# Optimization experiments

Measured on AMD Instinct MI355X. Metric: run time of the kernel, lower is better.

## Reference

```python
import jax, jax.numpy as jnp
import numpy as np

B, QLEN, MLEN, E, H, DH = 2, 1024, 1024, 1024, 16, 64
KLEN = QLEN + MLEN
LN_EPS = 1e-3  # keras LayerNormalization default epsilon


def layer_norm(x, gamma, beta):
    mu = jnp.mean(x, axis=-1, keepdims=True)
    var = jnp.mean(jnp.square(x - mu), axis=-1, keepdims=True)
    return (x - mu) * jax.lax.rsqrt(var + LN_EPS) * gamma + beta


def rel_shift(x):
    # x: [B, H, q, k] -> standard Transformer-XL relative shift
    b, h, q, k = x.shape
    x = jnp.pad(x, ((0, 0), (0, 0), (0, 0), (1, 0)))
    x = x.reshape(b, h, k + 1, q)[:, :, 1:, :]
    return x.reshape(b, h, q, k)


def setup_inputs() -> dict:
    key = jax.random.key(0)
    ks = jax.random.split(key, 12)
    s = 0.02
    inp = {
        "w": jax.random.normal(ks[0], (B, QLEN, E), jnp.float32),
        "r": jax.random.normal(ks[1], (1, KLEN, E), jnp.float32),
        "member": jax.random.normal(ks[2], (B, MLEN, E), jnp.float32),
        # causal mask over concatenated keys: 1 = masked
        "attn_mask": (jnp.arange(KLEN)[None, :] > (jnp.arange(QLEN)[:, None] + MLEN)).astype(jnp.float32),
        "Wq": jax.random.normal(ks[3], (E, H * DH), jnp.float32) * s,
        "Wk": jax.random.normal(ks[4], (E, H * DH), jnp.float32) * s,
        "Wv": jax.random.normal(ks[5], (E, H * DH), jnp.float32) * s,
        "Wr": jax.random.normal(ks[6], (E, H * DH), jnp.float32) * s,
        "Wo": jax.random.normal(ks[7], (H * DH, E), jnp.float32) * s,
        "r_w_bias": jnp.zeros((H, DH), jnp.float32),
        "r_r_bias": jnp.zeros((H, DH), jnp.float32),
        "ln1_g": jnp.ones((E,), jnp.float32),
        "ln1_b": jnp.zeros((E,), jnp.float32),
        "W1": jax.random.normal(ks[8], (E, 4 * E), jnp.float32) * s,
        "W2": jax.random.normal(ks[9], (4 * E, E), jnp.float32) * s,
        "ln2_g": jnp.ones((E,), jnp.float32),
        "ln2_b": jnp.zeros((E,), jnp.float32),
    }
    return inp


def reference(w, r, member, attn_mask, Wq, Wk, Wv, Wr, Wo, r_w_bias, r_r_bias,
              ln1_g, ln1_b, W1, W2, ln2_g, ln2_b):
    b, qlen, e = w.shape
    h, dh = r_w_bias.shape
    cat = jnp.concatenate([member, w], axis=1)          # [B, klen, E]
    q = (cat @ Wq)[:, -qlen:]                           # [B, q, H*DH]
    k = cat @ Wk                                        # [B, klen, H*DH]
    v = cat @ Wv
    rp = (r @ Wr)[0]                                    # [klen, H*DH] (shared over batch)
    qh = q.reshape(b, qlen, h, dh)
    kh = k.reshape(b, -1, h, dh)
    vh = v.reshape(b, -1, h, dh)
    rh = rp.reshape(-1, h, dh)
    AC = jnp.einsum('bqhd,bkhd->bhqk', qh + r_w_bias, kh)
    BD = jnp.einsum('bqhd,khd->bhqk', qh + r_r_bias, rh)
    BD = rel_shift(BD)
    attn = (AC + BD) / jnp.sqrt(jnp.float32(e))         # note: scaled by sqrt(embed_size)
    m = attn_mask[None, None]                           # [1,1,q,klen]
    attn = attn * (1.0 - m) - 1e30 * m
    p = jax.nn.softmax(attn, axis=-1)
    o = jnp.einsum('bhqk,bkhd->bqhd', p, vh).reshape(b, qlen, h * dh)
    o = o @ Wo
    x = layer_norm(w + o, ln1_g, ln1_b)
    y = jax.nn.relu(x @ W1) @ W2
    return layer_norm(y + x, ln2_g, ln2_b)
```

## Files before the change

### kernel.cpp

```cpp
#include <hip/hip_runtime.h>
#include <hip/hip_bf16.h>
#include <stdint.h>

typedef __bf16 bf16x8 __attribute__((ext_vector_type(8)));
typedef float  f32x4  __attribute__((ext_vector_type(4)));

constexpr int BB   = 2;
constexpr int QL   = 1024;
constexpr int ML   = 1024;
constexpr int KL   = 2048;
constexpr int ED   = 1024;
constexpr int HH   = 16;
constexpr int FF   = 4096;
constexpr size_t MN = 2048u * 1024u;

__device__ __forceinline__ bf16x8 ld8(const __hip_bfloat16* p) {
    return *reinterpret_cast<const bf16x8*>(p);
}
__device__ __forceinline__ void st8(__hip_bfloat16* p, bf16x8 v) {
    *reinterpret_cast<bf16x8*>(p) = v;
}
__device__ __forceinline__ f32x4 mfma16(bf16x8 a, bf16x8 b, f32x4 c) {
    return __builtin_amdgcn_mfma_f32_16x16x32_bf16(a, b, c, 0, 0, 0);
}
__device__ __forceinline__ void async16(void* lds, const void* g) {
    __builtin_amdgcn_global_load_lds((__attribute__((address_space(1))) void*)g,
                                     (__attribute__((address_space(3))) void*)lds,
                                     16, 0, 0);
}

__global__ __launch_bounds__(256) void build_cat(const float* __restrict__ w,
                                                 const float* __restrict__ mem,
                                                 __hip_bfloat16* __restrict__ cat) {
    size_t t = (size_t)blockIdx.x * 256 + threadIdx.x;
    size_t g = t * 8;
    int b   = (int)(g >> 21);
    int rem = (int)(g & ((1u << 21) - 1));
    int j = rem >> 10, e = rem & 1023;
    const float* src = (j < ML) ? &mem[((size_t)b * ML + j) * ED + e]
                                : &w[((size_t)b * QL + (j - ML)) * ED + e];
    float4 f0 = *(const float4*)src;
    float4 f1 = *(const float4*)(src + 4);
    union { bf16x8 v; __hip_bfloat16 h[8]; } u;
    u.h[0] = __float2bfloat16(f0.x); u.h[1] = __float2bfloat16(f0.y);
    u.h[2] = __float2bfloat16(f0.z); u.h[3] = __float2bfloat16(f0.w);
    u.h[4] = __float2bfloat16(f1.x); u.h[5] = __float2bfloat16(f1.y);
    u.h[6] = __float2bfloat16(f1.z); u.h[7] = __float2bfloat16(f1.w);
    st8(&cat[g], u.v);
}

__global__ __launch_bounds__(256) void cast8(const float* __restrict__ in,
                                             __hip_bfloat16* __restrict__ out) {
    size_t g = ((size_t)blockIdx.x * 256 + threadIdx.x) * 8;
    float4 f0 = *(const float4*)&in[g];
    float4 f1 = *(const float4*)&in[g + 4];
    union { bf16x8 v; __hip_bfloat16 h[8]; } u;
    u.h[0] = __float2bfloat16(f0.x); u.h[1] = __float2bfloat16(f0.y);
    u.h[2] = __float2bfloat16(f0.z); u.h[3] = __float2bfloat16(f0.w);
    u.h[4] = __float2bfloat16(f1.x); u.h[5] = __float2bfloat16(f1.y);
    u.h[6] = __float2bfloat16(f1.z); u.h[7] = __float2bfloat16(f1.w);
    st8(&out[g], u.v);
}

__global__ __launch_bounds__(256) void transpose_cast(const float* __restrict__ in,
                                                      __hip_bfloat16* __restrict__ out,
                                                      int K, int N) {
    __shared__ float tile[32][33];
    const int tx = threadIdx.x & 31, ty = threadIdx.x >> 5;
    const int n0 = blockIdx.x * 32, k0 = blockIdx.y * 32;
#pragma unroll
    for (int i = 0; i < 4; ++i)
        tile[ty + i * 8][tx] = in[(size_t)(k0 + ty + i * 8) * N + n0 + tx];
    __syncthreads();
#pragma unroll
    for (int i = 0; i < 4; ++i)
        out[(size_t)(n0 + ty + i * 8) * K + k0 + tx] = __float2bfloat16(tile[tx][ty + i * 8]);
}

__global__ __launch_bounds__(256) void transpose_v(const __hip_bfloat16* __restrict__ v,
                                                   __hip_bfloat16* __restrict__ vt) {
    __shared__ __hip_bfloat16 tile[32][33];
    const int tx = threadIdx.x & 31, ty = threadIdx.x >> 5;
    const int s = blockIdx.z, b = s >> 4, h = s & 15;
    const int j0 = blockIdx.x * 32, d0 = blockIdx.y * 32;
#pragma unroll
    for (int i = 0; i < 4; ++i)
        tile[ty + i * 8][tx] =
            v[((size_t)b * KL + j0 + ty + i * 8) * 1024 + h * 64 + d0 + tx];
    __syncthreads();
#pragma unroll
    for (int i = 0; i < 4; ++i)
        vt[((size_t)s * 64 + d0 + ty + i * 8) * KL + j0 + tx] = tile[tx][ty + i * 8];
}

template <int EPI, bool SK>
__global__ __launch_bounds__(256) void gemm_bt(const __hip_bfloat16* __restrict__ A,
                                               const __hip_bfloat16* __restrict__ Bt,
                                               void* __restrict__ Cv,
                                               int N, int kLen, int lda, int ldb) {
    __shared__ __align__(16) __hip_bfloat16 sA[128 * 32];
    __shared__ __align__(16) __hip_bfloat16 sB[128 * 32];
    const int tid = threadIdx.x;
    const int lane = tid & 63;
    const int l16 = lane & 15, quad = lane >> 4;
    const int wv = tid >> 6;
    const int wm = wv >> 1, wn = wv & 1;
    const int bm = blockIdx.y * 128, bn = blockIdx.x * 128;
    const int kOff = SK ? blockIdx.z * kLen : 0;
    const int c0 = tid, c1 = 256 + tid;
    const int r0 = c0 >> 2, o0 = (c0 & 3) * 8;
    const int r1 = c1 >> 2, o1 = (c1 & 3) * 8;
    f32x4 acc[4][4] = {};
    for (int k0 = 0; k0 < kLen; k0 += 32) {
        async16(&sA[c0 * 8], A + (size_t)(bm + r0) * lda + kOff + k0 + o0);
        async16(&sA[c1 * 8], A + (size_t)(bm + r1) * lda + kOff + k0 + o1);
        async16(&sB[c0 * 8], Bt + (size_t)(bn + r0) * ldb + kOff + k0 + o0);
        async16(&sB[c1 * 8], Bt + (size_t)(bn + r1) * ldb + kOff + k0 + o1);
        __syncthreads();
        bf16x8 af[4], bfr[4];
#pragma unroll
        for (int i = 0; i < 4; ++i)
            af[i] = ld8(&sA[(wm * 64 + i * 16 + l16) * 32 + quad * 8]);
#pragma unroll
        for (int j = 0; j < 4; ++j)
            bfr[j] = ld8(&sB[(wn * 64 + j * 16 + l16) * 32 + quad * 8]);
#pragma unroll
        for (int i = 0; i < 4; ++i)
#pragma unroll
            for (int j = 0; j < 4; ++j)
                acc[i][j] = mfma16(af[i], bfr[j], acc[i][j]);
        __syncthreads();
    }
#pragma unroll
    for (int i = 0; i < 4; ++i)
#pragma unroll
        for (int j = 0; j < 4; ++j)
#pragma unroll
            for (int rg = 0; rg < 4; ++rg) {
                size_t row = bm + wm * 64 + i * 16 + quad * 4 + rg;
                size_t col = bn + wn * 64 + j * 16 + l16;
                float v = acc[i][j][rg];
                if (EPI == 0) {
                    float* C = (float*)Cv + (SK ? (size_t)blockIdx.z * MN : 0);
                    C[row * N + col] = v;
                } else {
                    __hip_bfloat16* C = (__hip_bfloat16*)Cv;
                    C[row * N + col] = __float2bfloat16(fmaxf(v, 0.f));
                }
            }
}

__global__ __launch_bounds__(256) void gemm_qkv(const __hip_bfloat16* __restrict__ A,
                                                const __hip_bfloat16* __restrict__ Bt,
                                                __hip_bfloat16* __restrict__ qwb,
                                                __hip_bfloat16* __restrict__ qrb,
                                                __hip_bfloat16* __restrict__ kbuf,
                                                __hip_bfloat16* __restrict__ vbuf,
                                                const float* __restrict__ rwb,
                                                const float* __restrict__ rrb) {
    const int bm = blockIdx.y * 128, bn = blockIdx.x * 128;
    const int region = blockIdx.x >> 3;
    if (region == 0 && (bm & 2047) < 1024) return;
    __shared__ __align__(16) __hip_bfloat16 sA[128 * 32];
    __shared__ __align__(16) __hip_bfloat16 sB[128 * 32];
    const int tid = threadIdx.x;
    const int lane = tid & 63;
    const int l16 = lane & 15, quad = lane >> 4;
    const int wv = tid >> 6;
    const int wm = wv >> 1, wn = wv & 1;
    const int c0 = tid, c1 = 256 + tid;
    const int r0 = c0 >> 2, o0 = (c0 & 3) * 8;
    const int r1 = c1 >> 2, o1 = (c1 & 3) * 8;
    f32x4 acc[4][4] = {};
    for (int k0 = 0; k0 < 1024; k0 += 32) {
        async16(&sA[c0 * 8], A + (size_t)(bm + r0) * 1024 + k0 + o0);
        async16(&sA[c1 * 8], A + (size_t)(bm + r1) * 1024 + k0 + o1);
        async16(&sB[c0 * 8], Bt + (size_t)(bn + r0) * 1024 + k0 + o0);
        async16(&sB[c1 * 8], Bt + (size_t)(bn + r1) * 1024 + k0 + o1);
        __syncthreads();
        bf16x8 af[4], bfr[4];
#pragma unroll
        for (int i = 0; i < 4; ++i)
            af[i] = ld8(&sA[(wm * 64 + i * 16 + l16) * 32 + quad * 8]);
#pragma unroll
        for (int j = 0; j < 4; ++j)
            bfr[j] = ld8(&sB[(wn * 64 + j * 16 + l16) * 32 + quad * 8]);
#pragma unroll
        for (int i = 0; i < 4; ++i)
#pragma unroll
            for (int j = 0; j < 4; ++j)
                acc[i][j] = mfma16(af[i], bfr[j], acc[i][j]);
        __syncthreads();
    }
#pragma unroll
    for (int j = 0; j < 4; ++j) {
        const int col = bn + wn * 64 + j * 16 + l16;
        float bw = 0.f, br = 0.f;
        if (region == 0) { bw = rwb[col]; br = rrb[col]; }
#pragma unroll
        for (int i = 0; i < 4; ++i)
#pragma unroll
            for (int rg = 0; rg < 4; ++rg) {
                const int row = bm + wm * 64 + i * 16 + quad * 4 + rg;
                const int bb = row >> 11, jr = row & 2047;
                float v = acc[i][j][rg];
                if (region == 0) {
                    size_t o = ((size_t)(bb * 1024 + (jr - 1024))) * 1024 + col;
                    qwb[o] = __float2bfloat16(v + bw);
                    qrb[o] = __float2bfloat16(v + br);
                } else if (region == 1) {
                    kbuf[((size_t)(bb * 2048 + jr)) * 1024 + (col - 1024)] = __float2bfloat16(v);
                } else {
                    vbuf[((size_t)(bb * 2048 + jr)) * 1024 + (col - 2048)] = __float2bfloat16(v);
                }
            }
    }
}

__global__ __launch_bounds__(128, 2) void flash_attn2(
        const __hip_bfloat16* __restrict__ qw, const __hip_bfloat16* __restrict__ qr,
        const __hip_bfloat16* __restrict__ kbuf, const __hip_bfloat16* __restrict__ vtb,
        const __hip_bfloat16* __restrict__ rpb,
        float* __restrict__ Opart, float* __restrict__ lpart) {
    __shared__ __align__(16) __hip_bfloat16 sk[64][72];
    __shared__ __align__(16) __hip_bfloat16 srp[128][72];
    __shared__ __align__(16) __hip_bfloat16 spb[2][32][72];
    const int tid = threadIdx.x, wv = tid >> 6, lane = tid & 63;
    const int l16 = lane & 15, quad = lane >> 4;
    const int qb = blockIdx.x >> 1, chunk = blockIdx.x & 1;
    const int h = blockIdx.y, b = blockIdx.z;
    const int i0b = qb * 64, i0w = i0b + wv * 32;

    bf16x8 qaw[2][2], qar[2][2];
#pragma unroll
    for (int g = 0; g < 2; ++g)
#pragma unroll
        for (int kf = 0; kf < 2; ++kf) {
            size_t qi = ((size_t)(b * QL + i0w + g * 16 + l16)) * 1024 + h * 64 + kf * 32 + quad * 8;
            qaw[g][kf] = ld8(&qw[qi]);
            qar[g][kf] = ld8(&qr[qi]);
        }
    f32x4 oacc[2][4] = {};
    f32x4 lacc[2] = {};
    union { bf16x8 v; __hip_bfloat16 h8[8]; } ou;
#pragma unroll
    for (int j = 0; j < 8; ++j) ou.h8[j] = __float2bfloat16(l16 == 0 ? 1.f : 0.f);
    const bf16x8 onesf = ou.v;

    int srcIdx[4], selr[4];
#pragma unroll
    for (int r = 0; r < 4; ++r) {
        int s = l16 + 15 - (quad * 4 + r);
        selr[r] = s >> 4;
        srcIdx[r] = (lane & 48) | (s & 15);
    }
    const int T = qb + 17, Ta = T >> 1;
    const int t0 = chunk ? Ta : 0, t1 = chunk ? T : Ta;
    const int rbase = 32 - wv * 32;

    for (int jt = t0; jt < t1; ++jt) {
        const int j0 = jt * 64;
        const int ub = j0 - i0b + 960;
#pragma unroll
        for (int p = 0; p < 4; ++p) {
            int cc = p * 128 + tid, row = cc >> 3, off = (cc & 7) * 8;
            st8(&sk[row][off], ld8(&kbuf[((size_t)(b * KL + j0 + row)) * 1024 + h * 64 + off]));
        }
#pragma unroll
        for (int p = 0; p < 8; ++p) {
            int cc = p * 128 + tid, row = cc >> 3, off = (cc & 7) * 8;
            int u = ub + row;
            if (u < KL) {
                st8(&srp[row][off], ld8(&rpb[(size_t)u * 1024 + h * 64 + off]));
            } else {
                union { bf16x8 v; uint32_t w[4]; } z;
                z.w[0] = z.w[1] = z.w[2] = z.w[3] = 0u;
                st8(&srp[row][off], z.v);
            }
        }
        bf16x8 vvf[4][2];
#pragma unroll
        for (int dt = 0; dt < 4; ++dt) {
            size_t vr = ((size_t)((b * HH + h) * 64 + dt * 16 + l16)) * 2048 + j0 + quad * 8;
            vvf[dt][0] = ld8(&vtb[vr]);
            vvf[dt][1] = ld8(&vtb[vr + 32]);
        }
        __syncthreads();
        f32x4 sfr[2][4];
#pragma unroll
        for (int nt = 0; nt < 4; ++nt) {
            bf16x8 b0 = ld8(&sk[nt * 16 + l16][quad * 8]);
            bf16x8 b1 = ld8(&sk[nt * 16 + l16][32 + quad * 8]);
#pragma unroll
            for (int g = 0; g < 2; ++g) {
                f32x4 z = {};
                z = mfma16(qaw[g][0], b0, z);
                z = mfma16(qaw[g][1], b1, z);
                sfr[g][nt] = z;
            }
        }
        bf16x8 bF0[6], bF1[6];
#pragma unroll
        for (int t = 0; t < 6; ++t) {
            int rr = rbase + t * 16 + l16;
            bF0[t] = ld8(&srp[rr][quad * 8]);
            bF1[t] = ld8(&srp[rr][32 + quad * 8]);
        }
#pragma unroll
        for (int g = 0; g < 2; ++g) {
            f32x4 bd[5];
#pragma unroll
            for (int t = 0; t < 5; ++t) {
                int ts = t + 1 - g;
                f32x4 z = {};
                z = mfma16(qar[g][0], bF0[ts], z);
                z = mfma16(qar[g][1], bF1[ts], z);
                bd[t] = z;
            }
            float pre[5][4];
#pragma unroll
            for (int t = 0; t < 5; ++t)
#pragma unroll
                for (int r = 0; r < 4; ++r)
                    pre[t][r] = __shfl(bd[t][r], srcIdx[r], 64);
#pragma unroll
            for (int nt = 0; nt < 4; ++nt)
#pragma unroll
                for (int r = 0; r < 4; ++r) {
                    float bdv = selr[r] ? pre[nt + 1][r] : pre[nt][r];
                    float sv = (sfr[g][nt][r] + bdv) * 0.03125f;
                    int ii = i0w + g * 16 + quad * 4 + r;
                    int jj = j0 + nt * 16 + l16;
                    float p = (jj <= ii + ML) ? __expf(sv) : 0.f;
                    spb[wv][g * 16 + quad * 4 + r][nt * 16 + l16] = __float2bfloat16(p);
                }
        }
#pragma unroll
        for (int g = 0; g < 2; ++g) {
            bf16x8 pa0 = ld8(&spb[wv][g * 16 + l16][quad * 8]);
            bf16x8 pa1 = ld8(&spb[wv][g * 16 + l16][32 + quad * 8]);
            lacc[g] = mfma16(pa0, onesf, lacc[g]);
            lacc[g] = mfma16(pa1, onesf, lacc[g]);
#pragma unroll
            for (int dt = 0; dt < 4; ++dt) {
                oacc[g][dt] = mfma16(pa0, vvf[dt][0], oacc[g][dt]);
                oacc[g][dt] = mfma16(pa1, vvf[dt][1], oacc[g][dt]);
            }
        }
        __syncthreads();
    }
    const size_t obase = ((size_t)((chunk * 2 + b) * HH + h)) * 1024 * 64;
#pragma unroll
    for (int g = 0; g < 2; ++g)
#pragma unroll
        for (int dt = 0; dt < 4; ++dt)
#pragma unroll
            for (int r = 0; r < 4; ++r) {
                int q = i0w + g * 16 + quad * 4 + r;
                Opart[obase + (size_t)q * 64 + dt * 16 + l16] = oacc[g][dt][r];
            }
    if (l16 == 0) {
        const size_t lbase = ((size_t)((chunk * 2 + b) * HH + h)) * 1024;
#pragma unroll
        for (int g = 0; g < 2; ++g)
#pragma unroll
            for (int r = 0; r < 4; ++r) {
                int q = i0w + g * 16 + quad * 4 + r;
                lpart[lbase + q] = lacc[g][r];
            }
    }
}

__global__ __launch_bounds__(256) void combine_attn(const float* __restrict__ Opart,
                                                    const float* __restrict__ lpart,
                                                    __hip_bfloat16* __restrict__ og) {
    size_t t = (size_t)blockIdx.x * 256 + threadIdx.x;
    size_t e4 = t * 4;
    int d  = (int)(e4 & 63);
    int q  = (int)((e4 >> 6) & 1023);
    int hh = (int)((e4 >> 16) & 15);
    int bb = (int)(e4 >> 20);
    size_t i0 = ((size_t)(bb * HH + hh) * 1024 + q) * 64 + d;
    const size_t CS = (size_t)2 * HH * 1024 * 64;
    float4 o0 = *(const float4*)&Opart[i0];
    float4 o1 = *(const float4*)&Opart[i0 + CS];
    float l0 = lpart[(size_t)(bb * HH + hh) * 1024 + q];
    float l1 = lpart[(size_t)(bb * HH + hh) * 1024 + q + 2 * HH * 1024];
    float inv = 1.f / (l0 + l1);
    union { __hip_bfloat16 h[4]; uint2 u; } o;
    o.h[0] = __float2bfloat16((o0.x + o1.x) * inv);
    o.h[1] = __float2bfloat16((o0.y + o1.y) * inv);
    o.h[2] = __float2bfloat16((o0.z + o1.z) * inv);
    o.h[3] = __float2bfloat16((o0.w + o1.w) * inv);
    *(uint2*)&og[((size_t)bb * 1024 + q) * 1024 + hh * 64 + d] = o.u;
}

__global__ __launch_bounds__(256) void combine_bf(const float* __restrict__ p,
                                                  __hip_bfloat16* __restrict__ out) {
    size_t g = ((size_t)blockIdx.x * 256 + threadIdx.x) * 8;
    float4 a0 = *(const float4*)&p[g];
    float4 a1 = *(const float4*)&p[g + 4];
    float4 b0 = *(const float4*)&p[g + MN];
    float4 b1 = *(const float4*)&p[g + MN + 4];
    union { bf16x8 v; __hip_bfloat16 h[8]; } u;
    u.h[0] = __float2bfloat16(a0.x + b0.x); u.h[1] = __float2bfloat16(a0.y + b0.y);
    u.h[2] = __float2bfloat16(a0.z + b0.z); u.h[3] = __float2bfloat16(a0.w + b0.w);
    u.h[4] = __float2bfloat16(a1.x + b1.x); u.h[5] = __float2bfloat16(a1.y + b1.y);
    u.h[6] = __float2bfloat16(a1.z + b1.z); u.h[7] = __float2bfloat16(a1.w + b1.w);
    st8(&out[g], u.v);
}

template <int NP, bool WB>
__global__ __launch_bounds__(256) void add_ln_k(const float* __restrict__ res,
                                                const float* __restrict__ parts,
                                                const float* __restrict__ gam,
                                                const float* __restrict__ bet,
                                                float* __restrict__ of,
                                                __hip_bfloat16* __restrict__ ob) {
    const int tid = threadIdx.x;
    const size_t base = (size_t)blockIdx.x * ED;
    const int col = tid * 4;
    float4 va = *(const float4*)&res[base + col];
    float x0 = va.x, x1 = va.y, x2 = va.z, x3 = va.w;
#pragma unroll
    for (int z = 0; z < NP; ++z) {
        float4 p = *(const float4*)&parts[(size_t)z * MN + base + col];
        x0 += p.x; x1 += p.y; x2 += p.z; x3 += p.w;
    }
    float s1 = x0 + x1 + x2 + x3;
    float s2 = x0 * x0 + x1 * x1 + x2 * x2 + x3 * x3;
    for (int o = 32; o > 0; o >>= 1) {
        s1 += __shfl_down(s1, o, 64);
        s2 += __shfl_down(s2, o, 64);
    }
    __shared__ float p1[4], p2[4];
    if ((tid & 63) == 0) { p1[tid >> 6] = s1; p2[tid >> 6] = s2; }
    __syncthreads();
    float S1 = p1[0] + p1[1] + p1[2] + p1[3];
    float S2 = p2[0] + p2[1] + p2[2] + p2[3];
    float mu = S1 * (1.0f / ED);
    float var = S2 * (1.0f / ED) - mu * mu;
    float rs = rsqrtf(var + 1e-3f);
    float4 g4 = *(const float4*)&gam[col];
    float4 b4 = *(const float4*)&bet[col];
    float y0 = (x0 - mu) * rs * g4.x + b4.x;
    float y1 = (x1 - mu) * rs * g4.y + b4.y;
    float y2 = (x2 - mu) * rs * g4.z + b4.z;
    float y3 = (x3 - mu) * rs * g4.w + b4.w;
    *(float4*)&of[base + col] = make_float4(y0, y1, y2, y3);
    if (WB) {
        ob[base + col + 0] = __float2bfloat16(y0);
        ob[base + col + 1] = __float2bfloat16(y1);
        ob[base + col + 2] = __float2bfloat16(y2);
        ob[base + col + 3] = __float2bfloat16(y3);
    }
}

extern "C" void kernel_launch(void* const* d_in, const int* in_sizes, int n_in,
                              void* d_out, int out_size, void* d_ws, size_t ws_size,
                              hipStream_t stream) {
    const float* w   = (const float*)d_in[0];
    const float* r   = (const float*)d_in[1];
    const float* mem = (const float*)d_in[2];
    const float* Wq  = (const float*)d_in[4];
    const float* Wk  = (const float*)d_in[5];
    const float* Wv  = (const float*)d_in[6];
    const float* Wr  = (const float*)d_in[7];
    const float* Wo  = (const float*)d_in[8];
    const float* rwb = (const float*)d_in[9];
    const float* rrb = (const float*)d_in[10];
    const float* g1  = (const float*)d_in[11];
    const float* b1  = (const float*)d_in[12];
    const float* W1  = (const float*)d_in[13];
    const float* W2  = (const float*)d_in[14];
    const float* g2  = (const float*)d_in[15];
    const float* b2  = (const float*)d_in[16];

    char* ws = (char*)d_ws;
    size_t off = 0;
    auto alloc = [&](size_t bytes) -> void* {
        void* p = ws + off;
        off += (bytes + 255) & ~(size_t)255;
        return p;
    };
    __hip_bfloat16* wqkvT = (__hip_bfloat16*)alloc((size_t)3072 * 1024 * 2);
    __hip_bfloat16* wrt   = (__hip_bfloat16*)alloc((size_t)ED * ED * 2);
    __hip_bfloat16* wot   = (__hip_bfloat16*)alloc((size_t)ED * ED * 2);
    __hip_bfloat16* w1t   = (__hip_bfloat16*)alloc((size_t)FF * ED * 2);
    __hip_bfloat16* w2t   = (__hip_bfloat16*)alloc((size_t)ED * FF * 2);
    __hip_bfloat16* qwb   = (__hip_bfloat16*)alloc((size_t)BB * QL * ED * 2);
    __hip_bfloat16* qrb   = (__hip_bfloat16*)alloc((size_t)BB * QL * ED * 2);
    __hip_bfloat16* vtb   = (__hip_bfloat16*)alloc((size_t)BB * KL * ED * 2);
    __hip_bfloat16* rpb   = (__hip_bfloat16*)alloc((size_t)KL * ED * 2);
    __hip_bfloat16* og    = (__hip_bfloat16*)alloc((size_t)BB * QL * ED * 2);
    char* regA = (char*)alloc((size_t)BB * KL * ED * 2);
    __hip_bfloat16* cat = (__hip_bfloat16*)regA;
    float*          xf  = (float*)regA;
    char* regB = (char*)alloc((size_t)KL * ED * 2);
    __hip_bfloat16* rbf = (__hip_bfloat16*)regB;
    __hip_bfloat16* xb  = (__hip_bfloat16*)regB;
    char* regC = (char*)alloc((size_t)BB * QL * FF * 2);
    __hip_bfloat16* kbuf = (__hip_bfloat16*)regC;
    __hip_bfloat16* vbuf = (__hip_bfloat16*)(regC + (size_t)BB * KL * ED * 2);
    __hip_bfloat16* y1   = (__hip_bfloat16*)regC;
    char* regD = (char*)alloc((size_t)2 * MN * 4);
    float* rp_part = (float*)regD;
    float* o_part  = (float*)regD;
    char* regE = (char*)alloc((size_t)4 * MN * 4 + (size_t)2 * BB * HH * QL * 4);
    float* Opart  = (float*)regE;
    float* lpart  = (float*)(regE + (size_t)2 * BB * HH * QL * 64 * 4);
    float* f_part = (float*)regE;
    if (off > ws_size) return;

    build_cat<<<2048, 256, 0, stream>>>(w, mem, cat);
    cast8<<<1024, 256, 0, stream>>>(r, rbf);
    transpose_cast<<<dim3(32, 32), 256, 0, stream>>>(Wq, wqkvT, 1024, 1024);
    transpose_cast<<<dim3(32, 32), 256, 0, stream>>>(Wk, wqkvT + (size_t)1024 * 1024, 1024, 1024);
    transpose_cast<<<dim3(32, 32), 256, 0, stream>>>(Wv, wqkvT + (size_t)2048 * 1024, 1024, 1024);
    transpose_cast<<<dim3(32, 32), 256, 0, stream>>>(Wr, wrt, 1024, 1024);
    transpose_cast<<<dim3(32, 32), 256, 0, stream>>>(Wo, wot, 1024, 1024);
    transpose_cast<<<dim3(128, 32), 256, 0, stream>>>(W1, w1t, 1024, 4096);
    transpose_cast<<<dim3(32, 128), 256, 0, stream>>>(W2, w2t, 4096, 1024);

    gemm_qkv<<<dim3(24, 32), 256, 0, stream>>>(cat, wqkvT, qwb, qrb, kbuf, vbuf, rwb, rrb);
    gemm_bt<0, true><<<dim3(8, 16, 2), 256, 0, stream>>>(rbf, wrt, rp_part, 1024, 512, 1024, 1024);
    combine_bf<<<1024, 256, 0, stream>>>(rp_part, rpb);
    transpose_v<<<dim3(64, 2, 32), 256, 0, stream>>>(vbuf, vtb);

    flash_attn2<<<dim3(32, 16, 2), 128, 0, stream>>>(qwb, qrb, kbuf, vtb, rpb, Opart, lpart);
    combine_attn<<<2048, 256, 0, stream>>>(Opart, lpart, og);

    gemm_bt<0, true><<<dim3(8, 16, 2), 256, 0, stream>>>(og, wot, o_part, 1024, 512, 1024, 1024);
    add_ln_k<2, true><<<2048, 256, 0, stream>>>(w, o_part, g1, b1, xf, xb);

    gemm_bt<2, false><<<dim3(32, 16, 1), 256, 0, stream>>>(xb, w1t, y1, 4096, 1024, 1024, 1024);
    gemm_bt<0, true><<<dim3(8, 16, 4), 256, 0, stream>>>(y1, w2t, f_part, 1024, 1024, 4096, 4096);
    add_ln_k<4, false><<<2048, 256, 0, stream>>>(xf, f_part, g2, b2, (float*)d_out, nullptr);
}
```

Baseline: 456.6 us.

## Fuse prep kernels, fold Wr projection into QKV GEMM, rework flash attention to single-wave blocks

```diff
diff --git a/kernel.cpp b/kernel.cpp
--- a/kernel.cpp
+++ b/kernel.cpp
@@ -29,16 +29,29 @@
                                      16, 0, 0);
 }
 
-__global__ __launch_bounds__(256) void build_cat(const float* __restrict__ w,
-                                                 const float* __restrict__ mem,
-                                                 __hip_bfloat16* __restrict__ cat) {
-    size_t t = (size_t)blockIdx.x * 256 + threadIdx.x;
-    size_t g = t * 8;
-    int b   = (int)(g >> 21);
-    int rem = (int)(g & ((1u << 21) - 1));
-    int j = rem >> 10, e = rem & 1023;
-    const float* src = (j < ML) ? &mem[((size_t)b * ML + j) * ED + e]
-                                : &w[((size_t)b * QL + (j - ML)) * ED + e];
+__global__ __launch_bounds__(256) void build_cat_r(const float* __restrict__ w,
+                                                   const float* __restrict__ mem,
+                                                   const float* __restrict__ r,
+                                                   __hip_bfloat16* __restrict__ cat,
+                                                   __hip_bfloat16* __restrict__ rbf) {
+    const int bx = blockIdx.x;
+    const float* src;
+    __hip_bfloat16* dst;
+    size_t g;
+    if (bx < 2048) {
+        size_t t = (size_t)bx * 256 + threadIdx.x;
+        g = t * 8;
+        int b   = (int)(g >> 21);
+        int rem = (int)(g & ((1u << 21) - 1));
+        int j = rem >> 10, e = rem & 1023;
+        src = (j < ML) ? &mem[((size_t)b * ML + j) * ED + e]
+                       : &w[((size_t)b * QL + (j - ML)) * ED + e];
+        dst = &cat[g];
+    } else {
+        g = ((size_t)(bx - 2048) * 256 + threadIdx.x) * 8;
+        src = &r[g];
+        dst = &rbf[g];
+    }
     float4 f0 = *(const float4*)src;
     float4 f1 = *(const float4*)(src + 4);
     union { bf16x8 v; __hip_bfloat16 h[8]; } u;
@@ -46,20 +59,7 @@
     u.h[2] = __float2bfloat16(f0.z); u.h[3] = __float2bfloat16(f0.w);
     u.h[4] = __float2bfloat16(f1.x); u.h[5] = __float2bfloat16(f1.y);
     u.h[6] = __float2bfloat16(f1.z); u.h[7] = __float2bfloat16(f1.w);
-    st8(&cat[g], u.v);
-}
-
-__global__ __launch_bounds__(256) void cast8(const float* __restrict__ in,
-                                             __hip_bfloat16* __restrict__ out) {
-    size_t g = ((size_t)blockIdx.x * 256 + threadIdx.x) * 8;
-    float4 f0 = *(const float4*)&in[g];
-    float4 f1 = *(const float4*)&in[g + 4];
-    union { bf16x8 v; __hip_bfloat16 h[8]; } u;
-    u.h[0] = __float2bfloat16(f0.x); u.h[1] = __float2bfloat16(f0.y);
-    u.h[2] = __float2bfloat16(f0.z); u.h[3] = __float2bfloat16(f0.w);
-    u.h[4] = __float2bfloat16(f1.x); u.h[5] = __float2bfloat16(f1.y);
-    u.h[6] = __float2bfloat16(f1.z); u.h[7] = __float2bfloat16(f1.w);
-    st8(&out[g], u.v);
+    st8(dst, u.v);
 }
 
 __global__ __launch_bounds__(256) void transpose_cast(const float* __restrict__ in,
@@ -75,6 +75,26 @@
 #pragma unroll
     for (int i = 0; i < 4; ++i)
         out[(size_t)(n0 + ty + i * 8) * K + k0 + tx] = __float2bfloat16(tile[tx][ty + i * 8]);
+}
+
+__global__ __launch_bounds__(256) void tc5(const float* __restrict__ s0, const float* __restrict__ s1,
+                                           const float* __restrict__ s2, const float* __restrict__ s3,
+                                           const float* __restrict__ s4,
+                                           __hip_bfloat16* __restrict__ wqkvT,
+                                           __hip_bfloat16* __restrict__ wot) {
+    __shared__ float tile[32][33];
+    const int z = blockIdx.z;
+    const float* in = (z == 0) ? s0 : (z == 1) ? s1 : (z == 2) ? s2 : (z == 3) ? s3 : s4;
+    __hip_bfloat16* out = (z == 4) ? wot : wqkvT + (size_t)z * 1024 * 1024;
+    const int tx = threadIdx.x & 31, ty = threadIdx.x >> 5;
+    const int n0 = blockIdx.x * 32, k0 = blockIdx.y * 32;
+#pragma unroll
+    for (int i = 0; i < 4; ++i)
+        tile[ty + i * 8][tx] = in[(size_t)(k0 + ty + i * 8) * 1024 + n0 + tx];
+    __syncthreads();
+#pragma unroll
+    for (int i = 0; i < 4; ++i)
+        out[(size_t)(n0 + ty + i * 8) * 1024 + k0 + tx] = __float2bfloat16(tile[tx][ty + i * 8]);
 }
 
 __global__ __launch_bounds__(256) void transpose_v(const __hip_bfloat16* __restrict__ v,
@@ -150,17 +170,21 @@
             }
 }
 
-__global__ __launch_bounds__(256) void gemm_qkv(const __hip_bfloat16* __restrict__ A,
-                                                const __hip_bfloat16* __restrict__ Bt,
-                                                __hip_bfloat16* __restrict__ qwb,
-                                                __hip_bfloat16* __restrict__ qrb,
-                                                __hip_bfloat16* __restrict__ kbuf,
-                                                __hip_bfloat16* __restrict__ vbuf,
-                                                const float* __restrict__ rwb,
-                                                const float* __restrict__ rrb) {
+__global__ __launch_bounds__(256) void gemm_qkvr(const __hip_bfloat16* __restrict__ cat,
+                                                 const __hip_bfloat16* __restrict__ rbf,
+                                                 const __hip_bfloat16* __restrict__ Bt,
+                                                 __hip_bfloat16* __restrict__ qwb,
+                                                 __hip_bfloat16* __restrict__ qrb,
+                                                 __hip_bfloat16* __restrict__ kbuf,
+                                                 __hip_bfloat16* __restrict__ vbuf,
+                                                 __hip_bfloat16* __restrict__ rpb,
+                                                 const float* __restrict__ rwb,
+                                                 const float* __restrict__ rrb) {
     const int bm = blockIdx.y * 128, bn = blockIdx.x * 128;
     const int region = blockIdx.x >> 3;
     if (region == 0 && (bm & 2047) < 1024) return;
+    if (region == 3 && bm >= 2048) return;
+    const __hip_bfloat16* A = (region == 3) ? rbf : cat;
     __shared__ __align__(16) __hip_bfloat16 sA[128 * 32];
     __shared__ __align__(16) __hip_bfloat16 sB[128 * 32];
     const int tid = threadIdx.x;
@@ -210,35 +234,35 @@
                     qrb[o] = __float2bfloat16(v + br);
                 } else if (region == 1) {
                     kbuf[((size_t)(bb * 2048 + jr)) * 1024 + (col - 1024)] = __float2bfloat16(v);
+                } else if (region == 2) {
+                    vbuf[((size_t)(bb * 2048 + jr)) * 1024 + (col - 2048)] = __float2bfloat16(v);
                 } else {
-                    vbuf[((size_t)(bb * 2048 + jr)) * 1024 + (col - 2048)] = __float2bfloat16(v);
+                    rpb[(size_t)row * 1024 + (col - 3072)] = __float2bfloat16(v);
                 }
             }
     }
 }
 
-__global__ __launch_bounds__(128, 2) void flash_attn2(
+__global__ __launch_bounds__(64, 3) void flash_attn3(
         const __hip_bfloat16* __restrict__ qw, const __hip_bfloat16* __restrict__ qr,
         const __hip_bfloat16* __restrict__ kbuf, const __hip_bfloat16* __restrict__ vtb,
         const __hip_bfloat16* __restrict__ rpb,
         float* __restrict__ Opart, float* __restrict__ lpart) {
-    __shared__ __align__(16) __hip_bfloat16 sk[64][72];
-    __shared__ __align__(16) __hip_bfloat16 srp[128][72];
-    __shared__ __align__(16) __hip_bfloat16 spb[2][32][72];
-    const int tid = threadIdx.x, wv = tid >> 6, lane = tid & 63;
+    __shared__ __align__(16) __hip_bfloat16 spb[32][76];
+    const int lane = threadIdx.x;
     const int l16 = lane & 15, quad = lane >> 4;
-    const int qb = blockIdx.x >> 1, chunk = blockIdx.x & 1;
+    const int qi = blockIdx.x >> 1, chunk = blockIdx.x & 1;
     const int h = blockIdx.y, b = blockIdx.z;
-    const int i0b = qb * 64, i0w = i0b + wv * 32;
+    const int i0 = qi * 32;
 
     bf16x8 qaw[2][2], qar[2][2];
 #pragma unroll
     for (int g = 0; g < 2; ++g)
 #pragma unroll
         for (int kf = 0; kf < 2; ++kf) {
-            size_t qi = ((size_t)(b * QL + i0w + g * 16 + l16)) * 1024 + h * 64 + kf * 32 + quad * 8;
-            qaw[g][kf] = ld8(&qw[qi]);
-            qar[g][kf] = ld8(&qr[qi]);
+            size_t qi_ = ((size_t)(b * QL + i0 + g * 16 + l16)) * 1024 + h * 64 + kf * 32 + quad * 8;
+            qaw[g][kf] = ld8(&qw[qi_]);
+            qar[g][kf] = ld8(&qr[qi_]);
         }
     f32x4 oacc[2][4] = {};
     f32x4 lacc[2] = {};
@@ -252,45 +276,22 @@
     for (int r = 0; r < 4; ++r) {
         int s = l16 + 15 - (quad * 4 + r);
         selr[r] = s >> 4;
-        srcIdx[r] = (lane & 48) | (s & 15);
-    }
-    const int T = qb + 17, Ta = T >> 1;
+        srcIdx[r] = (quad * 16) | (s & 15);
+    }
+    const int T = (i0 + 1119) >> 6, Ta = T >> 1;
     const int t0 = chunk ? Ta : 0, t1 = chunk ? T : Ta;
-    const int rbase = 32 - wv * 32;
+    const __hip_bfloat16* kB = kbuf + (size_t)b * KL * 1024 + h * 64;
+    const __hip_bfloat16* vB = vtb + ((size_t)(b * HH + h) * 64) * 2048;
+    const __hip_bfloat16* rB = rpb + h * 64;
 
     for (int jt = t0; jt < t1; ++jt) {
         const int j0 = jt * 64;
-        const int ub = j0 - i0b + 960;
-#pragma unroll
-        for (int p = 0; p < 4; ++p) {
-            int cc = p * 128 + tid, row = cc >> 3, off = (cc & 7) * 8;
-            st8(&sk[row][off], ld8(&kbuf[((size_t)(b * KL + j0 + row)) * 1024 + h * 64 + off]));
-        }
-#pragma unroll
-        for (int p = 0; p < 8; ++p) {
-            int cc = p * 128 + tid, row = cc >> 3, off = (cc & 7) * 8;
-            int u = ub + row;
-            if (u < KL) {
-                st8(&srp[row][off], ld8(&rpb[(size_t)u * 1024 + h * 64 + off]));
-            } else {
-                union { bf16x8 v; uint32_t w[4]; } z;
-                z.w[0] = z.w[1] = z.w[2] = z.w[3] = 0u;
-                st8(&srp[row][off], z.v);
-            }
-        }
-        bf16x8 vvf[4][2];
-#pragma unroll
-        for (int dt = 0; dt < 4; ++dt) {
-            size_t vr = ((size_t)((b * HH + h) * 64 + dt * 16 + l16)) * 2048 + j0 + quad * 8;
-            vvf[dt][0] = ld8(&vtb[vr]);
-            vvf[dt][1] = ld8(&vtb[vr + 32]);
-        }
-        __syncthreads();
         f32x4 sfr[2][4];
 #pragma unroll
         for (int nt = 0; nt < 4; ++nt) {
-            bf16x8 b0 = ld8(&sk[nt * 16 + l16][quad * 8]);
-            bf16x8 b1 = ld8(&sk[nt * 16 + l16][32 + quad * 8]);
+            const __hip_bfloat16* kr = kB + (size_t)(j0 + nt * 16 + l16) * 1024 + quad * 8;
+            bf16x8 b0 = ld8(kr);
+            bf16x8 b1 = ld8(kr + 32);
 #pragma unroll
             for (int g = 0; g < 2; ++g) {
                 f32x4 z = {};
@@ -299,64 +300,76 @@
                 sfr[g][nt] = z;
             }
         }
-        bf16x8 bF0[6], bF1[6];
-#pragma unroll
-        for (int t = 0; t < 6; ++t) {
-            int rr = rbase + t * 16 + l16;
-            bF0[t] = ld8(&srp[rr][quad * 8]);
-            bF1[t] = ld8(&srp[rr][32 + quad * 8]);
+        f32x4 bd[2][5];
+        const int ubase = j0 - i0 + 992;
+#pragma unroll
+        for (int s = 0; s < 6; ++s) {
+            int row = ubase + s * 16 + l16;
+            if (row > 2047) row = 2047;
+            const __hip_bfloat16* rr = rB + (size_t)row * 1024 + quad * 8;
+            bf16x8 f0 = ld8(rr);
+            bf16x8 f1 = ld8(rr + 32);
+            if (s >= 1) {
+                f32x4 z = {};
+                z = mfma16(qar[0][0], f0, z);
+                z = mfma16(qar[0][1], f1, z);
+                bd[0][s - 1] = z;
+            }
+            if (s <= 4) {
+                f32x4 z = {};
+                z = mfma16(qar[1][0], f0, z);
+                z = mfma16(qar[1][1], f1, z);
+                bd[1][s] = z;
+            }
         }
 #pragma unroll
         for (int g = 0; g < 2; ++g) {
-            f32x4 bd[5];
-#pragma unroll
-            for (int t = 0; t < 5; ++t) {
-                int ts = t + 1 - g;
-                f32x4 z = {};
-                z = mfma16(qar[g][0], bF0[ts], z);
-                z = mfma16(qar[g][1], bF1[ts], z);
-                bd[t] = z;
-            }
             float pre[5][4];
 #pragma unroll
             for (int t = 0; t < 5; ++t)
 #pragma unroll
                 for (int r = 0; r < 4; ++r)
-                    pre[t][r] = __shfl(bd[t][r], srcIdx[r], 64);
+                    pre[t][r] = __shfl(bd[g][t][r], srcIdx[r], 64);
 #pragma unroll
             for (int nt = 0; nt < 4; ++nt)
 #pragma unroll
                 for (int r = 0; r < 4; ++r) {
                     float bdv = selr[r] ? pre[nt + 1][r] : pre[nt][r];
                     float sv = (sfr[g][nt][r] + bdv) * 0.03125f;
-                    int ii = i0w + g * 16 + quad * 4 + r;
+                    int ii = i0 + g * 16 + quad * 4 + r;
                     int jj = j0 + nt * 16 + l16;
                     float p = (jj <= ii + ML) ? __expf(sv) : 0.f;
-                    spb[wv][g * 16 + quad * 4 + r][nt * 16 + l16] = __float2bfloat16(p);
+                    spb[g * 16 + quad * 4 + r][nt * 16 + l16] = __float2bfloat16(p);
                 }
         }
+        bf16x8 pa[2][2];
 #pragma unroll
         for (int g = 0; g < 2; ++g) {
-            bf16x8 pa0 = ld8(&spb[wv][g * 16 + l16][quad * 8]);
-            bf16x8 pa1 = ld8(&spb[wv][g * 16 + l16][32 + quad * 8]);
-            lacc[g] = mfma16(pa0, onesf, lacc[g]);
-            lacc[g] = mfma16(pa1, onesf, lacc[g]);
-#pragma unroll
-            for (int dt = 0; dt < 4; ++dt) {
-                oacc[g][dt] = mfma16(pa0, vvf[dt][0], oacc[g][dt]);
-                oacc[g][dt] = mfma16(pa1, vvf[dt][1], oacc[g][dt]);
-            }
+            pa[g][0] = ld8(&spb[g * 16 + l16][quad * 8]);
+            pa[g][1] = ld8(&spb[g * 16 + l16][32 + quad * 8]);
+            lacc[g] = mfma16(pa[g][0], onesf, lacc[g]);
+            lacc[g] = mfma16(pa[g][1], onesf, lacc[g]);
         }
-        __syncthreads();
-    }
-    const size_t obase = ((size_t)((chunk * 2 + b) * HH + h)) * 1024 * 64;
+#pragma unroll
+        for (int dt = 0; dt < 4; ++dt) {
+            const __hip_bfloat16* vr = vB + (size_t)(dt * 16 + l16) * 2048 + j0 + quad * 8;
+            bf16x8 v0 = ld8(vr);
+            bf16x8 v1 = ld8(vr + 32);
+#pragma unroll
+            for (int g = 0; g < 2; ++g) {
+                oacc[g][dt] = mfma16(pa[g][0], v0, oacc[g][dt]);
+                oacc[g][dt] = mfma16(pa[g][1], v1, oacc[g][dt]);
+            }
+        }
+    }
+    const size_t obase = ((size_t)((chunk * 2 + b) * HH + h)) * (1024 * 64);
 #pragma unroll
     for (int g = 0; g < 2; ++g)
 #pragma unroll
         for (int dt = 0; dt < 4; ++dt)
 #pragma unroll
             for (int r = 0; r < 4; ++r) {
-                int q = i0w + g * 16 + quad * 4 + r;
+                int q = i0 + g * 16 + quad * 4 + r;
                 Opart[obase + (size_t)q * 64 + dt * 16 + l16] = oacc[g][dt][r];
             }
     if (l16 == 0) {
@@ -365,7 +378,7 @@
         for (int g = 0; g < 2; ++g)
 #pragma unroll
             for (int r = 0; r < 4; ++r) {
-                int q = i0w + g * 16 + quad * 4 + r;
+                int q = i0 + g * 16 + quad * 4 + r;
                 lpart[lbase + q] = lacc[g][r];
             }
     }
@@ -395,21 +408,6 @@
     *(uint2*)&og[((size_t)bb * 1024 + q) * 1024 + hh * 64 + d] = o.u;
 }
 
-__global__ __launch_bounds__(256) void combine_bf(const float* __restrict__ p,
-                                                  __hip_bfloat16* __restrict__ out) {
-    size_t g = ((size_t)blockIdx.x * 256 + threadIdx.x) * 8;
-    float4 a0 = *(const float4*)&p[g];
-    float4 a1 = *(const float4*)&p[g + 4];
-    float4 b0 = *(const float4*)&p[g + MN];
-    float4 b1 = *(const float4*)&p[g + MN + 4];
-    union { bf16x8 v; __hip_bfloat16 h[8]; } u;
-    u.h[0] = __float2bfloat16(a0.x + b0.x); u.h[1] = __float2bfloat16(a0.y + b0.y);
-    u.h[2] = __float2bfloat16(a0.z + b0.z); u.h[3] = __float2bfloat16(a0.w + b0.w);
-    u.h[4] = __float2bfloat16(a1.x + b1.x); u.h[5] = __float2bfloat16(a1.y + b1.y);
-    u.h[6] = __float2bfloat16(a1.z + b1.z); u.h[7] = __float2bfloat16(a1.w + b1.w);
-    st8(&out[g], u.v);
-}
-
 template <int NP, bool WB>
 __global__ __launch_bounds__(256) void add_ln_k(const float* __restrict__ res,
                                                 const float* __restrict__ parts,
@@ -483,8 +481,7 @@
         off += (bytes + 255) & ~(size_t)255;
         return p;
     };
-    __hip_bfloat16* wqkvT = (__hip_bfloat16*)alloc((size_t)3072 * 1024 * 2);
-    __hip_bfloat16* wrt   = (__hip_bfloat16*)alloc((size_t)ED * ED * 2);
+    __hip_bfloat16* wqkvT = (__hip_bfloat16*)alloc((size_t)4096 * 1024 * 2);
     __hip_bfloat16* wot   = (__hip_bfloat16*)alloc((size_t)ED * ED * 2);
     __hip_bfloat16* w1t   = (__hip_bfloat16*)alloc((size_t)FF * ED * 2);
     __hip_bfloat16* w2t   = (__hip_bfloat16*)alloc((size_t)ED * FF * 2);
@@ -503,35 +500,27 @@
     __hip_bfloat16* kbuf = (__hip_bfloat16*)regC;
     __hip_bfloat16* vbuf = (__hip_bfloat16*)(regC + (size_t)BB * KL * ED * 2);
     __hip_bfloat16* y1   = (__hip_bfloat16*)regC;
-    char* regD = (char*)alloc((size_t)2 * MN * 4);
-    float* rp_part = (float*)regD;
-    float* o_part  = (float*)regD;
-    char* regE = (char*)alloc((size_t)4 * MN * 4 + (size_t)2 * BB * HH * QL * 4);
+    char* regE = (char*)alloc((size_t)4 * MN * 4);
     float* Opart  = (float*)regE;
     float* lpart  = (float*)(regE + (size_t)2 * BB * HH * QL * 64 * 4);
+    float* o_part = (float*)regE;
     float* f_part = (float*)regE;
     if (off > ws_size) return;
 
-    build_cat<<<2048, 256, 0, stream>>>(w, mem, cat);
-    cast8<<<1024, 256, 0, stream>>>(r, rbf);
-    transpose_cast<<<dim3(32, 32), 256, 0, stream>>>(Wq, wqkvT, 1024, 1024);
-    transpose_cast<<<dim3(32, 32), 256, 0, stream>>>(Wk, wqkvT + (size_t)1024 * 1024, 1024, 1024);
-    transpose_cast<<<dim3(32, 32), 256, 0, stream>>>(Wv, wqkvT + (size_t)2048 * 1024, 1024, 1024);
-    transpose_cast<<<dim3(32, 32), 256, 0, stream>>>(Wr, wrt, 1024, 1024);
-    transpose_cast<<<dim3(32, 32), 256, 0, stream>>>(Wo, wot, 1024, 1024);
+    build_cat_r<<<3072, 256, 0, stream>>>(w, mem, r, cat, rbf);
+    tc5<<<dim3(32, 32, 5), 256, 0, stream>>>(Wq, Wk, Wv, Wr, Wo, wqkvT, wot);
     transpose_cast<<<dim3(128, 32), 256, 0, stream>>>(W1, w1t, 1024, 4096);
     transpose_cast<<<dim3(32, 128), 256, 0, stream>>>(W2, w2t, 4096, 1024);
 
-    gemm_qkv<<<dim3(24, 32), 256, 0, stream>>>(cat, wqkvT, qwb, qrb, kbuf, vbuf, rwb, rrb);
-    gemm_bt<0, true><<<dim3(8, 16, 2), 256, 0, stream>>>(rbf, wrt, rp_part, 1024, 512, 1024, 1024);
-    combine_bf<<<1024, 256, 0, stream>>>(rp_part, rpb);
+    gemm_qkvr<<<dim3(32, 32), 256, 0, stream>>>(cat, rbf, wqkvT, qwb, qrb, kbuf, vbuf, rpb,
+                                                rwb, rrb);
     transpose_v<<<dim3(64, 2, 32), 256, 0, stream>>>(vbuf, vtb);
 
-    flash_attn2<<<dim3(32, 16, 2), 128, 0, stream>>>(qwb, qrb, kbuf, vtb, rpb, Opart, lpart);
+    flash_attn3<<<dim3(64, 16, 2), 64, 0, stream>>>(qwb, qrb, kbuf, vtb, rpb, Opart, lpart);
     combine_attn<<<2048, 256, 0, stream>>>(Opart, lpart, og);
 
-    gemm_bt<0, true><<<dim3(8, 16, 2), 256, 0, stream>>>(og, wot, o_part, 1024, 512, 1024, 1024);
-    add_ln_k<2, true><<<2048, 256, 0, stream>>>(w, o_part, g1, b1, xf, xb);
+    gemm_bt<0, true><<<dim3(8, 16, 4), 256, 0, stream>>>(og, wot, o_part, 1024, 256, 1024, 1024);
+    add_ln_k<4, true><<<2048, 256, 0, stream>>>(w, o_part, g1, b1, xf, xb);
 
     gemm_bt<2, false><<<dim3(32, 16, 1), 256, 0, stream>>>(xb, w1t, y1, 4096, 1024, 1024, 1024);
     gemm_bt<0, true><<<dim3(8, 16, 4), 256, 0, stream>>>(y1, w2t, f_part, 1024, 1024, 4096, 4096);
```

New measurement: 443.6 us. 2.9% less time.
